# Performance work log

Hardware: AMD Instinct MI355X
Metric: run time of the kernel (lower is better)

The kernel has to match this reference:

```python
import jax, jax.numpy as jnp
import numpy as np

MAX_CH = 21
LAT_DIM = 64
D_EMBED = 1024
N_HEADS = 16
D_HEAD = D_EMBED // N_HEADS  # 64
L = MAX_CH * LAT_DIM         # 1344 latents
B, T = 4, 1024


def setup_inputs() -> dict:
    key = jax.random.key(0)
    k1, k2, k3, k4, k5, k6 = jax.random.split(key, 6)
    x = jax.random.normal(k1, (B, T, D_EMBED), dtype=jnp.float32)
    # boolean channel mask [b, L, T]
    ch_mask = jax.random.randint(k2, (B, L, T), 0, 2) > 0
    # learned latent queries [L, H*d] (xavier-uniform-ish init)
    lim_q = float(np.sqrt(6.0 / (L + N_HEADS * D_HEAD)))
    latent_q = jax.random.uniform(k3, (L, N_HEADS * D_HEAD), minval=-lim_q, maxval=lim_q, dtype=jnp.float32)
    # Linear weights (torch layout: [out, in]) and biases
    lim_w = float(np.sqrt(1.0 / D_EMBED))
    w_k_w = jax.random.uniform(k4, (N_HEADS * D_HEAD, D_EMBED), minval=-lim_w, maxval=lim_w, dtype=jnp.float32)
    w_k_b = jnp.zeros((N_HEADS * D_HEAD,), dtype=jnp.float32)
    w_v_w = jax.random.uniform(k5, (N_HEADS * D_HEAD, D_EMBED), minval=-lim_w, maxval=lim_w, dtype=jnp.float32)
    w_v_b = jax.random.uniform(k6, (N_HEADS * D_HEAD,), minval=-lim_w, maxval=lim_w, dtype=jnp.float32)
    return {"x": x, "ch_mask": ch_mask, "latent_q": latent_q,
            "w_k_w": w_k_w, "w_k_b": w_k_b, "w_v_w": w_v_w, "w_v_b": w_v_b}


def reference(x, ch_mask, latent_q, w_k_w, w_k_b, w_v_w, w_v_b):
    b, t, d = x.shape
    H, dh = N_HEADS, D_HEAD
    l = latent_q.shape[0]
    # faithful to torch .view(-1, H, L, d): raw row-major reinterpretation
    lq = latent_q.reshape(1, H, l, dh)                    # [1,H,L,dh]
    k = (x @ w_k_w.T + w_k_b).reshape(b, t, H, dh).transpose(0, 2, 3, 1)  # [b,H,dh,T]
    v = (x @ w_v_w.T + w_v_b).reshape(b, t, H, dh).transpose(0, 2, 1, 3)  # [b,H,T,dh]
    scale = jnp.float32(H) ** -0.5  # note: n_heads**-0.5, as in source
    scores = jnp.einsum('ohld,bhdt->bhlt', lq, k) * scale  # [b,H,L,T]
    mask = ch_mask[:, None, :, :]                           # [b,1,L,T] broadcast over heads
    scores = jnp.where(mask, scores, jnp.float32(-1e9))
    w = jax.nn.softmax(scores, axis=-1)
    w = jnp.where(mask, w, jnp.float32(0.0))
    out = jnp.einsum('bhlt,bhtd->bhld', w, v)               # [b,H,L,dh]
    return out.transpose(0, 2, 1, 3).reshape(b, l, H * dh)  # [b,L,H*dh]
```

## Files before the change

kernel.cpp:

```cpp
#include <hip/hip_runtime.h>
#include <hip/hip_bf16.h>

#define B_SZ 4
#define T_SZ 1024
#define NH 16
#define L_SZ 1344
#define LT_COUNT 21

typedef __attribute__((ext_vector_type(8))) short short8;
typedef __attribute__((ext_vector_type(4))) short short4v;
typedef __attribute__((ext_vector_type(4))) float floatx4;

typedef __attribute__((address_space(1))) const void gvoid;
typedef __attribute__((address_space(3))) void svoid;
#define GLD16(gp, lp) \
  __builtin_amdgcn_global_load_lds((gvoid*)(gp), (svoid*)(lp), 16, 0, 0)

static __device__ inline short bf16bits(float f) {
  return __builtin_bit_cast(short, __float2bfloat16(f));
}
static __device__ inline short4v cvt4(float4 v) {
  short4v r;
  r.x = bf16bits(v.x); r.y = bf16bits(v.y);
  r.z = bf16bits(v.z); r.w = bf16bits(v.w);
  return r;
}

static __device__ inline unsigned pack_bf16_2(float a, float b) {
  unsigned ua = __builtin_bit_cast(unsigned, a) + 0x8000u;
  unsigned ub = __builtin_bit_cast(unsigned, b) + 0x8000u;
  return __builtin_amdgcn_perm(ub, ua, 0x07060302u);
}
static __device__ inline uint2 pack_bf16_4(float4 v) {
  return make_uint2(pack_bf16_2(v.x, v.y), pack_bf16_2(v.z, v.w));
}


__global__ __launch_bounds__(256) void mask_detect(
    const unsigned char* __restrict__ m, int* __restrict__ flag) {
  __shared__ int any_off4, any_at4;
  if (threadIdx.x == 0) { any_off4 = 0; any_at4 = 0; }
  __syncthreads();
  int a1 = 0, a2 = 0;
  for (int i = threadIdx.x; i < 4096; i += 256) {
    unsigned char v = m[i];
    if (v) {
      if ((i & 3) != 0) a1 = 1;
      if ((i & 7) == 4) a2 = 1;
    }
  }
  if (a1) atomicOr(&any_off4, 1);
  if (a2) atomicOr(&any_at4, 1);
  __syncthreads();
  if (threadIdx.x == 0) *flag = any_off4 ? 1 : (any_at4 ? 0 : 2);
}

__global__ __launch_bounds__(256) void prep_kernel(
    const float4* __restrict__ x, const float4* __restrict__ wk,
    const float4* __restrict__ wv,
    uint2* __restrict__ xb, uint2* __restrict__ wkb, uint2* __restrict__ wvb,
    const void* __restrict__ mask, const int* __restrict__ flag,
    unsigned int* __restrict__ bits) {
  int bid = blockIdx.x;
  if (bid < 6144) {
    size_t i = (size_t)bid * 256 + threadIdx.x;
    if (i < 1048576)      xb[i] = pack_bf16_4(x[i]);
    else if (i < 1310720) wkb[i - 1048576] = pack_bf16_4(wk[i - 1048576]);
    else                  wvb[i - 1310720] = pack_bf16_4(wv[i - 1310720]);
  } else {
    int idx = (bid - 6144) * 256 + threadIdx.x;
    int f = *flag;
    bool v;
    if (f == 1)      v = ((const signed char*)mask)[idx] != 0;
    else if (f == 2) v = ((const long long*)mask)[idx] != 0;
    else             v = ((const int*)mask)[idx] != 0;
    unsigned long long bal = __ballot(v);
    int lane = threadIdx.x & 63;
    if ((lane & 31) == 0) {
      unsigned int w = (lane & 32) ? (unsigned int)(bal >> 32) : (unsigned int)bal;
      bits[idx >> 5] = w;
    }
  }
}

__global__ __launch_bounds__(256, 4) void gemm_kv_bf16(
    const __hip_bfloat16* __restrict__ xb,
    const __hip_bfloat16* __restrict__ wkb, const __hip_bfloat16* __restrict__ wvb,
    const float* __restrict__ bk, const float* __restrict__ bv,
    __hip_bfloat16* __restrict__ k_buf, __hip_bfloat16* __restrict__ v_buf) {
  __shared__ __align__(16) __hip_bfloat16 ldsA[2][128 * 32];
  __shared__ __align__(16) __hip_bfloat16 ldsB[2][64 * 32];
  const int tid = threadIdx.x;
  const int lane = tid & 63, w = tid >> 6;
  const int wm = w & 1, wn = w >> 1;
  const int c15 = lane & 15, kq = lane >> 4;

  const __hip_bfloat16* A;
  const __hip_bfloat16* B;
  int TA, TB;
  if (blockIdx.z == 0) {
    A = wkb; B = xb; TA = blockIdx.x >> 6; TB = blockIdx.x & 63;
  } else {
    A = xb; B = wvb; TA = blockIdx.x >> 4; TB = blockIdx.x & 15;
  }
  const __hip_bfloat16* Abase = A + (size_t)TA * 128 * 1024;
  const __hip_bfloat16* Bbase = B + (size_t)TB * 64 * 1024;

  floatx4 acc[4][2];
  #pragma unroll
  for (int i = 0; i < 4; ++i)
    #pragma unroll
    for (int j = 0; j < 2; ++j) acc[i][j] = (floatx4){0.f, 0.f, 0.f, 0.f};

#define GSTAGE(sb, kk) do {                                                  \
    int cA_ = w * 128 + lane;                                                \
    int rA_ = cA_ >> 2, gA_ = (cA_ & 3) ^ (rA_ & 3);                         \
    GLD16(Abase + (size_t)rA_ * 1024 + (kk) + gA_ * 8,                       \
          &ldsA[sb][(w * 128) * 8]);                                         \
    int cA2_ = cA_ + 64;                                                     \
    int rA2_ = cA2_ >> 2, gA2_ = (cA2_ & 3) ^ (rA2_ & 3);                    \
    GLD16(Abase + (size_t)rA2_ * 1024 + (kk) + gA2_ * 8,                     \
          &ldsA[sb][(w * 128 + 64) * 8]);                                    \
    int cB_ = w * 64 + lane;                                                 \
    int rB_ = cB_ >> 2, gB_ = (cB_ & 3) ^ (rB_ & 3);                         \
    GLD16(Bbase + (size_t)rB_ * 1024 + (kk) + gB_ * 8,                       \
          &ldsB[sb][(w * 64) * 8]);                                          \
  } while (0)

  GSTAGE(0, 0);
  for (int kk = 0; kk < 1024; kk += 32) {
    const int buf = (kk >> 5) & 1;
    if (kk + 32 < 1024) {
      GSTAGE(buf ^ 1, kk + 32);
      asm volatile("s_waitcnt vmcnt(3)" ::: "memory");
    } else {
      asm volatile("s_waitcnt vmcnt(0)" ::: "memory");
    }
    __builtin_amdgcn_s_barrier();

    short8 af[4], bfr[2];
    #pragma unroll
    for (int mi = 0; mi < 4; ++mi) {
      int row = wm * 64 + mi * 16 + c15;
      af[mi] = *(const short8*)(&ldsA[buf][row * 32 + ((kq ^ (row & 3)) * 8)]);
    }
    #pragma unroll
    for (int ni = 0; ni < 2; ++ni) {
      int row = wn * 32 + ni * 16 + c15;
      bfr[ni] = *(const short8*)(&ldsB[buf][row * 32 + ((kq ^ (row & 3)) * 8)]);
    }
    #pragma unroll
    for (int mi = 0; mi < 4; ++mi)
      #pragma unroll
      for (int ni = 0; ni < 2; ++ni)
        acc[mi][ni] = __builtin_amdgcn_mfma_f32_16x16x32_bf16(
            af[mi], bfr[ni], acc[mi][ni], 0, 0, 0);

    asm volatile("s_waitcnt lgkmcnt(0)" ::: "memory");
    __builtin_amdgcn_s_barrier();
  }
#undef GSTAGE

  if (blockIdx.z == 0) {
    #pragma unroll
    for (int ni = 0; ni < 2; ++ni) {
      int gr = TB * 64 + wn * 32 + ni * 16 + c15;
      int b = gr >> 10, tc = (gr >> 6) & 15;
      int ni2 = (gr & 63) >> 4;
      #pragma unroll
      for (int mi = 0; mi < 4; ++mi) {
        int d0 = TA * 128 + wm * 64 + mi * 16 + kq * 4;
        int h = d0 >> 6, hd = d0 & 63;
        int half = hd >> 5, q4 = (hd >> 3) & 3, jlo = hd & 7;
        int bh = b * 16 + h;
        float4 b4 = *(const float4*)(bk + d0);
        float4 v4 = {acc[mi][ni][0] + b4.x, acc[mi][ni][1] + b4.y,
                     acc[mi][ni][2] + b4.z, acc[mi][ni][3] + b4.w};
        *(uint2*)(k_buf + ((size_t)((bh * 16 + tc) * 8 + ni2 * 2 + half)) * 512 +
                  (q4 * 16 + c15) * 8 + jlo) = pack_bf16_4(v4);
      }
    }
  } else {
    #pragma unroll
    for (int ni = 0; ni < 2; ++ni) {
      int d = TB * 64 + wn * 32 + ni * 16 + c15;
      int h = d >> 6;
      int di = (d & 63) >> 4;
      float bias = bv[d];
      #pragma unroll
      for (int mi = 0; mi < 4; ++mi) {
        int gr = TA * 128 + wm * 64 + mi * 16 + kq * 4;
        int b = gr >> 10, tc = (gr >> 6) & 15;
        int tl = gr & 63;
        int half = tl >> 5, q4 = (tl >> 3) & 3, jlo = tl & 7;
        int bh = b * 16 + h;
        float4 v4 = {acc[mi][ni][0] + bias, acc[mi][ni][1] + bias,
                     acc[mi][ni][2] + bias, acc[mi][ni][3] + bias};
        *(uint2*)(v_buf + ((size_t)((bh * 16 + tc) * 8 + di * 2 + half)) * 512 +
                  (q4 * 16 + c15) * 8 + jlo) = pack_bf16_4(v4);
      }
    }
  }
}

__global__ __launch_bounds__(256, 3) void attn_kernel(
    const float* __restrict__ latent_q,
    const __hip_bfloat16* __restrict__ k_buf,
    const __hip_bfloat16* __restrict__ v_buf,
    const unsigned int* __restrict__ mbits,
    float* __restrict__ out) {
  __shared__ __align__(16) __hip_bfloat16 ldsK[2][4096];
  __shared__ __align__(16) __hip_bfloat16 ldsV[2][4096];
  __shared__ __align__(16) __hip_bfloat16 pbuf[4][16 * 72];
  __shared__ uint2 mrows[64][17];

  const int tid = threadIdx.x;
  const int lane = tid & 63;
  const int w = tid >> 6;
  int bid = blockIdx.x;
  int xcd = bid & 7, j = bid >> 3;
  int bh = xcd * 8 + j / LT_COUNT;
  int lt = j % LT_COUNT;
  int h = bh & 15, b = bh >> 4;
  const int q4 = lane >> 4, c15 = lane & 15;
  const int l0 = lt * 64;

  {
    const unsigned int* msrc = mbits + (size_t)(b * L_SZ + l0) * 32;
    #pragma unroll
    for (int p = 0; p < 2; ++p) {
      int i = p * 256 + tid;
      uint4 m4 = *(const uint4*)(msrc + i * 4);
      int row = i >> 3, c2 = (i & 7) * 2;
      mrows[row][c2]     = make_uint2(m4.x, m4.y);
      mrows[row][c2 + 1] = make_uint2(m4.z, m4.w);
    }
  }

  const float QS = 0.25f * 1.44269504089f;
  short8 qf[2];
  {
    const float* qp = latent_q + ((size_t)(h * L_SZ + l0 + w * 16 + c15)) * 64 + q4 * 8;
    float4 a0 = *(const float4*)(qp);
    float4 a1 = *(const float4*)(qp + 4);
    float4 a2 = *(const float4*)(qp + 32);
    float4 a3 = *(const float4*)(qp + 36);
    a0.x *= QS; a0.y *= QS; a0.z *= QS; a0.w *= QS;
    a1.x *= QS; a1.y *= QS; a1.z *= QS; a1.w *= QS;
    a2.x *= QS; a2.y *= QS; a2.z *= QS; a2.w *= QS;
    a3.x *= QS; a3.y *= QS; a3.z *= QS; a3.w *= QS;
    short4v t0 = cvt4(a0), t1 = cvt4(a1), t2 = cvt4(a2), t3 = cvt4(a3);
    qf[0] = (short8){t0.x, t0.y, t0.z, t0.w, t1.x, t1.y, t1.z, t1.w};
    qf[1] = (short8){t2.x, t2.y, t2.z, t2.w, t3.x, t3.y, t3.z, t3.w};
  }
  __syncthreads();

  floatx4 l4 = (floatx4){0.f, 0.f, 0.f, 0.f};
  floatx4 o_acc[4];
  #pragma unroll
  for (int di = 0; di < 4; ++di) o_acc[di] = (floatx4){0.f, 0.f, 0.f, 0.f};

  const __hip_bfloat16* kb = k_buf + (size_t)bh * 65536;
  const __hip_bfloat16* vb = v_buf + (size_t)bh * 65536;
  __hip_bfloat16* pw = pbuf[w];

#define STAGE_KV(sb, tcn) do {                                              \
    const __hip_bfloat16* gk_ = kb + (size_t)(tcn) * 4096;                  \
    const __hip_bfloat16* gv_ = vb + (size_t)(tcn) * 4096;                  \
    int o0_ = w * 512 + lane * 8;                                           \
    GLD16(gk_ + o0_,        &ldsK[sb][w * 512]);                            \
    GLD16(gk_ + 2048 + o0_, &ldsK[sb][2048 + w * 512]);                     \
    GLD16(gv_ + o0_,        &ldsV[sb][w * 512]);                            \
    GLD16(gv_ + 2048 + o0_, &ldsV[sb][2048 + w * 512]);                     \
  } while (0)

  STAGE_KV(0, 0);

  for (int tc = 0; tc < 16; ++tc) {
    const int buf = tc & 1;
    if (tc + 1 < 16) {
      STAGE_KV(buf ^ 1, tc + 1);
      asm volatile("s_waitcnt vmcnt(4)" ::: "memory");
    } else {
      asm volatile("s_waitcnt vmcnt(0)" ::: "memory");
    }
    __builtin_amdgcn_s_barrier();

    short8 kf[2][4];
    #pragma unroll
    for (int half = 0; half < 2; ++half)
      #pragma unroll
      for (int ni = 0; ni < 4; ++ni)
        kf[half][ni] = *(const short8*)(&ldsK[buf][(ni * 2 + half) * 512 + lane * 8]);
    uint2 mw = mrows[w * 16 + c15][tc];
    floatx4 s[4];
    #pragma unroll
    for (int ni = 0; ni < 4; ++ni) s[ni] = (floatx4){0.f, 0.f, 0.f, 0.f};
    __builtin_amdgcn_s_setprio(1);
    #pragma unroll
    for (int half = 0; half < 2; ++half)
      #pragma unroll
      for (int ni = 0; ni < 4; ++ni)
        s[ni] = __builtin_amdgcn_mfma_f32_16x16x32_bf16(kf[half][ni], qf[half], s[ni], 0, 0, 0);
    __builtin_amdgcn_s_setprio(0);

    short8 vf[2][4];
    #pragma unroll
    for (int half = 0; half < 2; ++half)
      #pragma unroll
      for (int di = 0; di < 4; ++di)
        vf[half][di] = *(const short8*)(&ldsV[buf][(di * 2 + half) * 512 + lane * 8]);

    #pragma unroll
    for (int ni = 0; ni < 4; ++ni) {
      unsigned mword = (ni >= 2) ? mw.y : mw.x;
      float4 p4;
      #pragma unroll
      for (int r = 0; r < 4; ++r) {
        float e = exp2f(s[ni][r]);
        int sh = (ni & 1) * 16 + q4 * 4 + r;
        ((float*)&p4)[r] = ((mword >> sh) & 1) ? e : 0.f;
      }
      l4[0] += p4.x; l4[1] += p4.y;
      l4[2] += p4.z; l4[3] += p4.w;
      *(uint2*)(pw + c15 * 72 + ni * 16 + q4 * 4) = pack_bf16_4(p4);
    }

    short8 pf0 = *(const short8*)(pw + c15 * 72 + q4 * 8);
    short8 pf1 = *(const short8*)(pw + c15 * 72 + 32 + q4 * 8);
    __builtin_amdgcn_s_setprio(1);
    #pragma unroll
    for (int di = 0; di < 4; ++di)
      o_acc[di] = __builtin_amdgcn_mfma_f32_16x16x32_bf16(vf[0][di], pf0, o_acc[di], 0, 0, 0);
    #pragma unroll
    for (int di = 0; di < 4; ++di)
      o_acc[di] = __builtin_amdgcn_mfma_f32_16x16x32_bf16(vf[1][di], pf1, o_acc[di], 0, 0, 0);
    __builtin_amdgcn_s_setprio(0);

    asm volatile("s_waitcnt lgkmcnt(0)" ::: "memory");
    __builtin_amdgcn_s_barrier();
  }
#undef STAGE_KV

  float la = (l4[0] + l4[1]) + (l4[2] + l4[3]);
  la += __shfl_xor(la, 16, 64);
  la += __shfl_xor(la, 32, 64);
  float inv = (la > 0.f) ? 1.f / la : 0.f;
  float* ob = out + ((size_t)(b * L_SZ + l0 + w * 16 + c15)) * 1024 + h * 64;
  #pragma unroll
  for (int di = 0; di < 4; ++di) {
    float4 o4 = {o_acc[di][0] * inv, o_acc[di][1] * inv,
                 o_acc[di][2] * inv, o_acc[di][3] * inv};
    *(float4*)(ob + di * 16 + q4 * 4) = o4;
  }
}

extern "C" void kernel_launch(void* const* d_in, const int* in_sizes, int n_in,
                              void* d_out, int out_size, void* d_ws, size_t ws_size,
                              hipStream_t stream) {
  const float* x      = (const float*)d_in[0];
  const void* ch_mask = d_in[1];
  const float* lq     = (const float*)d_in[2];
  const float* wk     = (const float*)d_in[3];
  const float* bk     = (const float*)d_in[4];
  const float* wv     = (const float*)d_in[5];
  const float* bv     = (const float*)d_in[6];
  float* out = (float*)d_out;

  char* ws = (char*)d_ws;
  unsigned int* mbits   = (unsigned int*)ws;
  int* flag             = (int*)(ws + 720896);
  __hip_bfloat16* k_buf = (__hip_bfloat16*)(ws + 786432);
  __hip_bfloat16* v_buf = (__hip_bfloat16*)(ws + 786432 + 8388608);

  __hip_bfloat16* xb  = (__hip_bfloat16*)d_out;
  __hip_bfloat16* wkb = xb + 4 * 1024 * 1024;
  __hip_bfloat16* wvb = wkb + 1024 * 1024;

  mask_detect<<<1, 256, 0, stream>>>((const unsigned char*)ch_mask, flag);
  prep_kernel<<<27648, 256, 0, stream>>>(
      (const float4*)x, (const float4*)wk, (const float4*)wv,
      (uint2*)xb, (uint2*)wkb, (uint2*)wvb,
      ch_mask, flag, mbits);
  gemm_kv_bf16<<<dim3(512, 1, 2), 256, 0, stream>>>(xb, wkb, wvb, bk, bv, k_buf, v_buf);

  attn_kernel<<<8 * 168, 256, 0, stream>>>(lq, k_buf, v_buf, mbits, out);
}
```

Baseline: 198.9 us.

## Grid-stride prep kernel, register-prefetch mask bits, swizzle P buffer, raise attn occupancy

The prep kernel becomes a grid-stride loop over a 2048-block grid instead of one block per 256 items, and reads the mask flag once per thread. In the attention kernel, the shared-memory mask staging and its block barrier are removed. Each lane now prefetches its next mask word straight from global memory into registers one tile ahead. The P scratch buffer switches from padded rows to an XOR-swizzled 64-wide layout, and launch bounds rise to 4 waves per SIMD. Together these aim to cut LDS use and bank conflicts and raise occupancy, at the risk of register spills and extra global loads per iteration.

```diff
diff --git a/kernel.cpp b/kernel.cpp
--- a/kernel.cpp
+++ b/kernel.cpp
@@ -61,24 +61,25 @@
     uint2* __restrict__ xb, uint2* __restrict__ wkb, uint2* __restrict__ wvb,
     const void* __restrict__ mask, const int* __restrict__ flag,
     unsigned int* __restrict__ bits) {
-  int bid = blockIdx.x;
-  if (bid < 6144) {
-    size_t i = (size_t)bid * 256 + threadIdx.x;
-    if (i < 1048576)      xb[i] = pack_bf16_4(x[i]);
-    else if (i < 1310720) wkb[i - 1048576] = pack_bf16_4(wk[i - 1048576]);
-    else                  wvb[i - 1310720] = pack_bf16_4(wv[i - 1310720]);
-  } else {
-    int idx = (bid - 6144) * 256 + threadIdx.x;
-    int f = *flag;
-    bool v;
-    if (f == 1)      v = ((const signed char*)mask)[idx] != 0;
-    else if (f == 2) v = ((const long long*)mask)[idx] != 0;
-    else             v = ((const int*)mask)[idx] != 0;
-    unsigned long long bal = __ballot(v);
-    int lane = threadIdx.x & 63;
-    if ((lane & 31) == 0) {
-      unsigned int w = (lane & 32) ? (unsigned int)(bal >> 32) : (unsigned int)bal;
-      bits[idx >> 5] = w;
+  const int f = *flag;
+  const int lane = threadIdx.x & 63;
+  for (int vb = blockIdx.x; vb < 27648; vb += gridDim.x) {
+    if (vb < 6144) {
+      size_t i = (size_t)vb * 256 + threadIdx.x;
+      if (i < 1048576)      xb[i] = pack_bf16_4(x[i]);
+      else if (i < 1310720) wkb[i - 1048576] = pack_bf16_4(wk[i - 1048576]);
+      else                  wvb[i - 1310720] = pack_bf16_4(wv[i - 1310720]);
+    } else {
+      int idx = (vb - 6144) * 256 + threadIdx.x;
+      bool v;
+      if (f == 1)      v = ((const signed char*)mask)[idx] != 0;
+      else if (f == 2) v = ((const long long*)mask)[idx] != 0;
+      else             v = ((const int*)mask)[idx] != 0;
+      unsigned long long bal = __ballot(v);
+      if ((lane & 31) == 0) {
+        unsigned int w = (lane & 32) ? (unsigned int)(bal >> 32) : (unsigned int)bal;
+        bits[idx >> 5] = w;
+      }
     }
   }
 }
@@ -203,7 +204,7 @@
   }
 }
 
-__global__ __launch_bounds__(256, 3) void attn_kernel(
+__global__ __launch_bounds__(256, 4) void attn_kernel(
     const float* __restrict__ latent_q,
     const __hip_bfloat16* __restrict__ k_buf,
     const __hip_bfloat16* __restrict__ v_buf,
@@ -211,8 +212,7 @@
     float* __restrict__ out) {
   __shared__ __align__(16) __hip_bfloat16 ldsK[2][4096];
   __shared__ __align__(16) __hip_bfloat16 ldsV[2][4096];
-  __shared__ __align__(16) __hip_bfloat16 pbuf[4][16 * 72];
-  __shared__ uint2 mrows[64][17];
+  __shared__ __align__(16) __hip_bfloat16 pbuf[4][1024];
 
   const int tid = threadIdx.x;
   const int lane = tid & 63;
@@ -223,19 +223,8 @@
   int lt = j % LT_COUNT;
   int h = bh & 15, b = bh >> 4;
   const int q4 = lane >> 4, c15 = lane & 15;
+  const int c7 = c15 & 7;
   const int l0 = lt * 64;
-
-  {
-    const unsigned int* msrc = mbits + (size_t)(b * L_SZ + l0) * 32;
-    #pragma unroll
-    for (int p = 0; p < 2; ++p) {
-      int i = p * 256 + tid;
-      uint4 m4 = *(const uint4*)(msrc + i * 4);
-      int row = i >> 3, c2 = (i & 7) * 2;
-      mrows[row][c2]     = make_uint2(m4.x, m4.y);
-      mrows[row][c2 + 1] = make_uint2(m4.z, m4.w);
-    }
-  }
 
   const float QS = 0.25f * 1.44269504089f;
   short8 qf[2];
@@ -253,7 +242,6 @@
     qf[0] = (short8){t0.x, t0.y, t0.z, t0.w, t1.x, t1.y, t1.z, t1.w};
     qf[1] = (short8){t2.x, t2.y, t2.z, t2.w, t3.x, t3.y, t3.z, t3.w};
   }
-  __syncthreads();
 
   floatx4 l4 = (floatx4){0.f, 0.f, 0.f, 0.f};
   floatx4 o_acc[4];
@@ -263,6 +251,7 @@
   const __hip_bfloat16* kb = k_buf + (size_t)bh * 65536;
   const __hip_bfloat16* vb = v_buf + (size_t)bh * 65536;
   __hip_bfloat16* pw = pbuf[w];
+  const unsigned int* mrow = mbits + ((size_t)(b * L_SZ + l0 + w * 16 + c15)) * 32;
 
 #define STAGE_KV(sb, tcn) do {                                              \
     const __hip_bfloat16* gk_ = kb + (size_t)(tcn) * 4096;                  \
@@ -275,6 +264,7 @@
   } while (0)
 
   STAGE_KV(0, 0);
+  uint2 mw_cur = *(const uint2*)(mrow);
 
   for (int tc = 0; tc < 16; ++tc) {
     const int buf = tc & 1;
@@ -286,13 +276,14 @@
     }
     __builtin_amdgcn_s_barrier();
 
+    uint2 mw_nxt = *(const uint2*)(mrow + (((tc + 1) & 15) * 2));
+
     short8 kf[2][4];
     #pragma unroll
     for (int half = 0; half < 2; ++half)
       #pragma unroll
       for (int ni = 0; ni < 4; ++ni)
         kf[half][ni] = *(const short8*)(&ldsK[buf][(ni * 2 + half) * 512 + lane * 8]);
-    uint2 mw = mrows[w * 16 + c15][tc];
     floatx4 s[4];
     #pragma unroll
     for (int ni = 0; ni < 4; ++ni) s[ni] = (floatx4){0.f, 0.f, 0.f, 0.f};
@@ -313,7 +304,7 @@
 
     #pragma unroll
     for (int ni = 0; ni < 4; ++ni) {
-      unsigned mword = (ni >= 2) ? mw.y : mw.x;
+      unsigned mword = (ni >= 2) ? mw_cur.y : mw_cur.x;
       float4 p4;
       #pragma unroll
       for (int r = 0; r < 4; ++r) {
@@ -323,11 +314,13 @@
       }
       l4[0] += p4.x; l4[1] += p4.y;
       l4[2] += p4.z; l4[3] += p4.w;
-      *(uint2*)(pw + c15 * 72 + ni * 16 + q4 * 4) = pack_bf16_4(p4);
-    }
-
-    short8 pf0 = *(const short8*)(pw + c15 * 72 + q4 * 8);
-    short8 pf1 = *(const short8*)(pw + c15 * 72 + 32 + q4 * 8);
+      int pc = (ni * 2 + (q4 >> 1)) ^ c7;
+      *(uint2*)(pw + c15 * 64 + pc * 8 + (q4 & 1) * 4) = pack_bf16_4(p4);
+    }
+
+    int pc0 = q4 ^ c7;
+    short8 pf0 = *(const short8*)(pw + c15 * 64 + pc0 * 8);
+    short8 pf1 = *(const short8*)(pw + c15 * 64 + (pc0 ^ 4) * 8);
     __builtin_amdgcn_s_setprio(1);
     #pragma unroll
     for (int di = 0; di < 4; ++di)
@@ -336,6 +329,8 @@
     for (int di = 0; di < 4; ++di)
       o_acc[di] = __builtin_amdgcn_mfma_f32_16x16x32_bf16(vf[1][di], pf1, o_acc[di], 0, 0, 0);
     __builtin_amdgcn_s_setprio(0);
+
+    mw_cur = mw_nxt;
 
     asm volatile("s_waitcnt lgkmcnt(0)" ::: "memory");
     __builtin_amdgcn_s_barrier();
@@ -378,7 +373,7 @@
   __hip_bfloat16* wvb = wkb + 1024 * 1024;
 
   mask_detect<<<1, 256, 0, stream>>>((const unsigned char*)ch_mask, flag);
-  prep_kernel<<<27648, 256, 0, stream>>>(
+  prep_kernel<<<2048, 256, 0, stream>>>(
       (const float4*)x, (const float4*)wk, (const float4*)wv,
       (uint2*)xb, (uint2*)wkb, (uint2*)wvb,
       ch_mask, flag, mbits);
```

Measured after the change: 192.8 us. -3.1%, faster.
